# Optimization experiments

Hardware: AMD Instinct MI355X
Metric: run time of the kernel (lower is better)

Reference implementation:

```python
import jax, jax.numpy as jnp
import numpy as np

B, N = 8, 256            # molecules, atoms per molecule (equal sizes)
BN = B * N               # total nodes
E = 16384                # total edges
H, NH, HD = 256, 8, 32   # hidden, heads, head_dim
VD = 8                   # (lmax+1)^2 - 1 with lmax=2
CUTOFF = 5.0


def setup_inputs() -> dict:
    key = jax.random.key(0)
    ks = jax.random.split(key, 24)
    s = 1.0 / np.sqrt(H)
    d_raw = jax.random.normal(ks[5], (E, VD), jnp.float32)
    d_ij = d_raw / (jnp.linalg.norm(d_raw, axis=1, keepdims=True) + 1e-8)
    return {
        'x': jax.random.normal(ks[0], (BN, H), jnp.float32),
        'vec': jax.random.normal(ks[1], (BN, VD, H), jnp.float32),
        'edge_index': jax.random.randint(ks[2], (2, E), 0, BN, jnp.int32),
        'r_ij': jax.random.uniform(ks[3], (E,), jnp.float32) * CUTOFF,
        'f_ij': jax.random.normal(ks[4], (E, H), jnp.float32),
        'd_ij': d_ij,
        'batch': jnp.arange(BN, dtype=jnp.int32) // N,
        'ln_w': jnp.ones((H,), jnp.float32),
        'ln_b': jnp.zeros((H,), jnp.float32),
        'Wq': jax.random.normal(ks[6], (H, H), jnp.float32) * s,
        'Wk': jax.random.normal(ks[7], (H, H), jnp.float32) * s,
        'Wv': jax.random.normal(ks[8], (H, H), jnp.float32) * s,
        'Wao': jax.random.normal(ks[9], (H, H), jnp.float32) * s,
        'Wvec': jax.random.normal(ks[10], (H, 2 * H), jnp.float32) * s,
        'Wdv': jax.random.normal(ks[11], (H, H), jnp.float32) * s,
        'bdv': jnp.zeros((H,), jnp.float32),
        'Ws': jax.random.normal(ks[12], (H, 2 * H), jnp.float32) * s,
        'bs': jnp.zeros((2 * H,), jnp.float32),
        'Wo': jax.random.normal(ks[13], (H, 3 * H), jnp.float32) * s,
        'bo': jnp.zeros((3 * H,), jnp.float32),
        'Wf': jax.random.normal(ks[14], (H, H), jnp.float32) * s,
        'bf': jnp.zeros((H,), jnp.float32),
        'Wsrc': jax.random.normal(ks[15], (H, H), jnp.float32) * s,
        'Wtrg': jax.random.normal(ks[16], (H, H), jnp.float32) * s,
    }


def _vector_rejection(v, d):
    # v: [E, VD, H], d: [E, VD]
    proj = (v * d[:, :, None]).sum(axis=1, keepdims=True)
    return v - proj * d[:, :, None]


def _layer(x, vec, edge_index, r_ij, f_ij, d_ij,
           ln_w, ln_b, Wq, Wk, Wv, Wao, Wvec, Wdv, bdv,
           Ws, bs, Wo, bo, Wf, bf, Wsrc, Wtrg):
    silu = jax.nn.silu
    # ---- LayerNorm on scalar features; VecLayerNorm('none', non-trainable) = identity
    mu = x.mean(-1, keepdims=True)
    var = ((x - mu) ** 2).mean(-1, keepdims=True)
    xn = (x - mu) / jnp.sqrt(var + 1e-5) * ln_w + ln_b

    # ---- 3-body padded attention (equal graph sizes -> mask is all-True)
    x_x = xn.reshape(B, N, H)
    q = (x_x @ Wq).reshape(B, N, NH, HD)
    k = (x_x @ Wk).reshape(B, N, NH, HD)
    vv = (x_x @ Wv).reshape(B, N, NH, HD)
    attn = silu(jnp.einsum('bihd,bjhd->bhij', q, k) / jnp.sqrt(jnp.float32(HD)))
    # mean over neighbor dim j fused into the contraction ( / N )
    v = (jnp.einsum('bhij,bjhd->bihd', attn, vv) / N).reshape(B, N, H) @ Wao
    v = v.reshape(BN, NH, HD)

    dv = silu(f_ij @ Wdv + bdv).reshape(E, NH, HD)
    vp = vec @ Wvec                       # [BN, VD, 2H]
    vec1, vec3 = vp[..., :H], vp[..., H:]
    vec_sum = vec1.sum(axis=1)            # [BN, H]

    # ---- message passing (source_to_target: gather at src, scatter-add at dst)
    src, dst = edge_index[0], edge_index[1]
    cut = 0.5 * (jnp.cos(jnp.pi * r_ij / CUTOFF) + 1.0) * (r_ij < CUTOFF)
    v_j = (v[src] * cut[:, None, None] * dv).reshape(E, H)
    s12 = silu(v_j @ Ws + bs)
    s1, s2 = s12[:, :H], s12[:, H:]
    vec_j = vec[src] * s1[:, None, :] + s2[:, None, :] * d_ij[:, :, None]
    x_agg = jax.ops.segment_sum(v_j, dst, num_segments=BN)
    vec_agg = jax.ops.segment_sum(vec_j, dst, num_segments=BN)

    o = x_agg @ Wo + bo
    o1, o2, o3 = o[:, :H], o[:, H:2 * H], o[:, 2 * H:]
    dx = vec_sum * o2 + o3
    dvec = vec3 * o1[:, None, :] + vec_agg

    # ---- edge update (not last layer)
    w1 = _vector_rejection(vec[dst] @ Wtrg, d_ij)
    w2 = _vector_rejection(vec[src] @ Wsrc, -d_ij)
    w_dot = (w1 * w2).sum(axis=1)         # [E, H]
    df_ij = silu(f_ij @ Wf + bf) * w_dot
    return dx, dvec, df_ij


def reference(x, vec, edge_index, r_ij, f_ij, d_ij, batch,
              ln_w, ln_b, Wq, Wk, Wv, Wao, Wvec, Wdv, bdv,
              Ws, bs, Wo, bo, Wf, bf, Wsrc, Wtrg):
    return _layer(x, vec, edge_index, r_ij, f_ij, d_ij,
                  ln_w, ln_b, Wq, Wk, Wv, Wao, Wvec, Wdv, bdv,
                  Ws, bs, Wo, bo, Wf, bf, Wsrc, Wtrg)
```

## Files before the change

kernel.cpp:

```cpp
#include <hip/hip_runtime.h>
#include <hip/hip_bf16.h>
#include <math.h>

typedef __hip_bfloat16 bf16;
#define DEV __device__ __forceinline__
DEV float silu_f(float x) { return x / (1.0f + __expf(-x)); }
DEV float toF(bf16 x) { return __bfloat162float(x); }
DEV void storeF(float* p, float v) { *p = v; }
DEV void storeF(bf16* p, float v) { *p = __float2bfloat16(v); }

constexpr int Bc = 8, Nc = 256, BNc = 2048, Ec = 16384;
constexpr int Hc = 256, NHc = 8, HDc = 32, VDc = 8;

typedef __attribute__((ext_vector_type(8))) short short8;
typedef __attribute__((ext_vector_type(4))) float floatx4;

DEV void async_copy16(const void* g, void* l) {
  __builtin_amdgcn_global_load_lds(
      (const __attribute__((address_space(1))) void*)g,
      (__attribute__((address_space(3))) void*)l, 16, 0, 0);
}

__global__ __launch_bounds__(1024) void csr_k(const int* __restrict__ ei,
                                              int* __restrict__ rowptr,
                                              int* __restrict__ eids) {
  __shared__ int deg[2048];
  __shared__ int cur[2048];
  __shared__ int ps[1024];
  __shared__ int rp[2048];
  int t = threadIdx.x;
  for (int i = t; i < 2048; i += 1024) { deg[i] = 0; cur[i] = 0; }
  __syncthreads();
  for (int e = t; e < Ec; e += 1024) atomicAdd(&deg[ei[Ec + e]], 1);
  __syncthreads();
  int s0 = deg[2 * t], s1 = deg[2 * t + 1];
  ps[t] = s0 + s1;
  __syncthreads();
  for (int off = 1; off < 1024; off <<= 1) {
    int v = (t >= off) ? ps[t - off] : 0;
    __syncthreads();
    ps[t] += v;
    __syncthreads();
  }
  int base = (t == 0) ? 0 : ps[t - 1];
  rp[2 * t] = base; rp[2 * t + 1] = base + s0;
  rowptr[2 * t] = base; rowptr[2 * t + 1] = base + s0;
  if (t == 1023) rowptr[2048] = Ec;
  __syncthreads();
  for (int e = t; e < Ec; e += 1024) {
    int d = ei[Ec + e];
    int p = atomicAdd(&cur[d], 1);
    eids[rp[d] + p] = e;
  }
}

struct WDesc { const float* in; bf16* out; int K, N; };
struct WAll { WDesc d[11]; };

__global__ __launch_bounds__(256) void wprep_all_k(WAll wa) {
  WDesc wd = wa.d[blockIdx.z];
  if ((int)blockIdx.y * 32 >= wd.N) return;
  __shared__ float t[32][33];
  int k0 = blockIdx.x * 32, n0 = blockIdx.y * 32;
  int tx = threadIdx.x & 31, ty = threadIdx.x >> 5;
#pragma unroll
  for (int i = 0; i < 32; i += 8)
    t[ty + i][tx] = wd.in[(size_t)(k0 + ty + i) * wd.N + n0 + tx];
  __syncthreads();
#pragma unroll
  for (int i = 0; i < 32; i += 8)
    wd.out[(size_t)(n0 + ty + i) * wd.K + k0 + tx] = __float2bfloat16(t[tx][ty + i]);
}

__global__ __launch_bounds__(256) void cvt2_k(const float* __restrict__ a,
                                              bf16* __restrict__ ao,
                                              const float* __restrict__ b,
                                              bf16* __restrict__ bo) {
  int blk = blockIdx.x;
  const float* in = (blk < 4096) ? a : b;
  bf16* out = (blk < 4096) ? ao : bo;
  int i = ((blk & 4095) * 256 + threadIdx.x) * 4;
  float4 v = *(const float4*)&in[i];
  union { bf16 x[4]; uint2 u; } o;
  o.x[0] = __float2bfloat16(v.x); o.x[1] = __float2bfloat16(v.y);
  o.x[2] = __float2bfloat16(v.z); o.x[3] = __float2bfloat16(v.w);
  *(uint2*)&out[i] = o.u;
}

__global__ __launch_bounds__(256) void ln_k(const float* __restrict__ x,
    const float* __restrict__ w, const float* __restrict__ b,
    bf16* __restrict__ xn) {
  int row = blockIdx.x, h = threadIdx.x;
  float v = x[(size_t)row * Hc + h];
  __shared__ float sm[256];
  sm[h] = v; __syncthreads();
  for (int s = 128; s > 0; s >>= 1) { if (h < s) sm[h] += sm[h + s]; __syncthreads(); }
  float mu = sm[0] * (1.0f / 256.0f);
  __syncthreads();
  float d = v - mu;
  sm[h] = d * d; __syncthreads();
  for (int s = 128; s > 0; s >>= 1) { if (h < s) sm[h] += sm[h + s]; __syncthreads(); }
  float var = sm[0] * (1.0f / 256.0f);
  float r = rsqrtf(var + 1e-5f);
  xn[(size_t)row * Hc + h] = __float2bfloat16(d * r * w[h] + b[h]);
}

template <int ACT, typename TC>
__global__ __launch_bounds__(256) void mgemm_k(
    const bf16* __restrict__ A, const bf16* __restrict__ Bt,
    const float* __restrict__ bias, TC* __restrict__ C,
    int M, int K, int N) {
  __shared__ bf16 Als[128 * 32];
  __shared__ bf16 Bls[128 * 32];
  int tid = threadIdx.x;
  int lane = tid & 63, w = tid >> 6;
  int m0 = blockIdx.x * 128, n0 = blockIdx.y * 128;
  int wm = (w & 1) * 64, wn = (w >> 1) * 64;
  int fm = lane & 15, g = lane >> 4;
  floatx4 acc[4][4] = {};
  for (int k0 = 0; k0 < K; k0 += 32) {
#pragma unroll
    for (int t = 0; t < 2; ++t) {
      int c = t * 256 + w * 64 + lane;
      int r = c >> 2, q = c & 3;
      bf16* ldsA = &Als[(t * 256 + w * 64) * 8 + lane * 8];
      bf16* ldsB = &Bls[(t * 256 + w * 64) * 8 + lane * 8];
      async_copy16(A + (size_t)(m0 + r) * K + k0 + q * 8, ldsA);
      async_copy16(Bt + (size_t)(n0 + r) * K + k0 + q * 8, ldsB);
    }
    __syncthreads();
    short8 af[4], bg[4];
#pragma unroll
    for (int i = 0; i < 4; ++i) {
      af[i] = *(const short8*)&Als[(wm + i * 16 + fm) * 32 + g * 8];
      bg[i] = *(const short8*)&Bls[(wn + i * 16 + fm) * 32 + g * 8];
    }
#pragma unroll
    for (int mi = 0; mi < 4; ++mi)
#pragma unroll
      for (int ni = 0; ni < 4; ++ni)
        acc[mi][ni] = __builtin_amdgcn_mfma_f32_16x16x32_bf16(
            af[mi], bg[ni], acc[mi][ni], 0, 0, 0);
    __syncthreads();
  }
#pragma unroll
  for (int mi = 0; mi < 4; ++mi) {
    int row0 = m0 + wm + mi * 16 + g * 4;
#pragma unroll
    for (int ni = 0; ni < 4; ++ni) {
      int col = n0 + wn + ni * 16 + fm;
      float bv = bias ? bias[col] : 0.0f;
#pragma unroll
      for (int r = 0; r < 4; ++r) {
        float v = acc[mi][ni][r] + bv;
        if (ACT) v = silu_f(v);
        storeF(&C[(size_t)(row0 + r) * N + col], v);
      }
    }
  }
}

__global__ __launch_bounds__(256) void gemm_dvfw_k(
    const bf16* __restrict__ A, const bf16* __restrict__ Bt,
    const float* __restrict__ bdv, const float* __restrict__ bf_,
    const int* __restrict__ ei, const float* __restrict__ r_ij,
    const float* __restrict__ vbuf,
    bf16* __restrict__ vj, bf16* __restrict__ fW) {
  constexpr int K = 256, N = 512;
  __shared__ bf16 Als[128 * 32];
  __shared__ bf16 Bls[128 * 32];
  int tid = threadIdx.x;
  int lane = tid & 63, w = tid >> 6;
  int m0 = blockIdx.x * 128, n0 = blockIdx.y * 128;
  int wm = (w & 1) * 64, wn = (w >> 1) * 64;
  int fm = lane & 15, g = lane >> 4;
  floatx4 acc[4][4] = {};
  for (int k0 = 0; k0 < K; k0 += 32) {
#pragma unroll
    for (int t = 0; t < 2; ++t) {
      int c = t * 256 + w * 64 + lane;
      int r = c >> 2, q = c & 3;
      bf16* ldsA = &Als[(t * 256 + w * 64) * 8 + lane * 8];
      bf16* ldsB = &Bls[(t * 256 + w * 64) * 8 + lane * 8];
      async_copy16(A + (size_t)(m0 + r) * K + k0 + q * 8, ldsA);
      async_copy16(Bt + (size_t)(n0 + r) * K + k0 + q * 8, ldsB);
    }
    __syncthreads();
    short8 af[4], bg[4];
#pragma unroll
    for (int i = 0; i < 4; ++i) {
      af[i] = *(const short8*)&Als[(wm + i * 16 + fm) * 32 + g * 8];
      bg[i] = *(const short8*)&Bls[(wn + i * 16 + fm) * 32 + g * 8];
    }
#pragma unroll
    for (int mi = 0; mi < 4; ++mi)
#pragma unroll
      for (int ni = 0; ni < 4; ++ni)
        acc[mi][ni] = __builtin_amdgcn_mfma_f32_16x16x32_bf16(
            af[mi], bg[ni], acc[mi][ni], 0, 0, 0);
    __syncthreads();
  }
  bool isVj = (n0 < 256);
#pragma unroll
  for (int mi = 0; mi < 4; ++mi) {
    int row0 = m0 + wm + mi * 16 + g * 4;
#pragma unroll
    for (int r = 0; r < 4; ++r) {
      int e = row0 + r;
      int src = 0; float cut = 0.f;
      if (isVj) {
        src = ei[e];
        float rr = r_ij[e];
        cut = (rr < 5.0f) ? 0.5f * (cosf(0.6283185307179586f * rr) + 1.0f) : 0.0f;
      }
#pragma unroll
      for (int ni = 0; ni < 4; ++ni) {
        int col = n0 + wn + ni * 16 + fm;
        if (isVj) {
          float v = silu_f(acc[mi][ni][r] + bdv[col]);
          vj[(size_t)e * 256 + col] =
              __float2bfloat16(vbuf[(size_t)src * 256 + col] * cut * v);
        } else {
          float v = silu_f(acc[mi][ni][r] + bf_[col - 256]);
          fW[(size_t)e * 256 + (col - 256)] = __float2bfloat16(v);
        }
      }
    }
  }
}

__global__ __launch_bounds__(256) void attn_mfma_k(
    const bf16* __restrict__ qkv, bf16* __restrict__ ob) {
  constexpr int QS = 768;
  int b = blockIdx.x >> 3, h = blockIdx.x & 7;
  int tid = threadIdx.x, lane = tid & 63, w = tid >> 6;
  int fm = lane & 15, g = lane >> 4;
  __shared__ bf16 Vt[32][264];
  __shared__ bf16 Ps[4][64][72];
  const bf16* qb = qkv + (size_t)b * 256 * QS + h * 32;
  const bf16* kb = qb + 256;
  const bf16* vb = qb + 512;
#pragma unroll
  for (int c = 0; c < 4; ++c) {
    int chunk = c * 256 + tid;
    int j = chunk >> 2, part = chunk & 3;
    union { short8 v; bf16 x[8]; } t;
    t.v = *(const short8*)(vb + (size_t)j * QS + part * 8);
#pragma unroll
    for (int i = 0; i < 8; ++i) Vt[part * 8 + i][j] = t.x[i];
  }
  __syncthreads();
  short8 af[4];
#pragma unroll
  for (int mi = 0; mi < 4; ++mi)
    af[mi] = *(const short8*)(qb + (size_t)(w * 64 + mi * 16 + fm) * QS + g * 8);
  floatx4 oacc[4][2] = {};
  for (int jt = 0; jt < 4; ++jt) {
#pragma unroll
    for (int ni = 0; ni < 4; ++ni) {
      short8 bg = *(const short8*)(kb + (size_t)(jt * 64 + ni * 16 + fm) * QS + g * 8);
#pragma unroll
      for (int mi = 0; mi < 4; ++mi) {
        floatx4 z = {0.f, 0.f, 0.f, 0.f};
        floatx4 s = __builtin_amdgcn_mfma_f32_16x16x32_bf16(af[mi], bg, z, 0, 0, 0);
#pragma unroll
        for (int r = 0; r < 4; ++r) {
          float v = silu_f(s[r] * 0.17677669529663687f);
          Ps[w][mi * 16 + g * 4 + r][ni * 16 + fm] = __float2bfloat16(v);
        }
      }
    }
#pragma unroll
    for (int kt = 0; kt < 2; ++kt) {
      short8 bv0 = *(const short8*)&Vt[fm][jt * 64 + kt * 32 + g * 8];
      short8 bv1 = *(const short8*)&Vt[16 + fm][jt * 64 + kt * 32 + g * 8];
#pragma unroll
      for (int mi = 0; mi < 4; ++mi) {
        short8 ap = *(const short8*)&Ps[w][mi * 16 + fm][kt * 32 + g * 8];
        oacc[mi][0] = __builtin_amdgcn_mfma_f32_16x16x32_bf16(ap, bv0, oacc[mi][0], 0, 0, 0);
        oacc[mi][1] = __builtin_amdgcn_mfma_f32_16x16x32_bf16(ap, bv1, oacc[mi][1], 0, 0, 0);
      }
    }
  }
#pragma unroll
  for (int mi = 0; mi < 4; ++mi)
#pragma unroll
    for (int ni = 0; ni < 2; ++ni)
#pragma unroll
      for (int r = 0; r < 4; ++r) {
        int row = w * 64 + mi * 16 + g * 4 + r;
        int d = ni * 16 + fm;
        ob[((size_t)(b * 256 + row)) * 256 + h * 32 + d] =
            __float2bfloat16(oacc[mi][ni][r] * (1.0f / 256.0f));
      }
}

__global__ __launch_bounds__(256) void xagg_k(const bf16* __restrict__ vj,
                                              const int* __restrict__ rowptr,
                                              const int* __restrict__ eids,
                                              bf16* __restrict__ xagg_bf) {
  int n = blockIdx.x, h = threadIdx.x;
  float acc = 0.f;
  int lo = rowptr[n], hi = rowptr[n + 1];
  for (int i = lo; i < hi; ++i) {
    int e = eids[i];
    acc += toF(vj[(size_t)e * Hc + h]);
  }
  xagg_bf[(size_t)n * Hc + h] = __float2bfloat16(acc);
}

__global__ __launch_bounds__(256) void dvec_agg_k(
    const bf16* __restrict__ vec_bf, const bf16* __restrict__ s12,
    const float* __restrict__ d_ij, const int* __restrict__ ei,
    const int* __restrict__ rowptr, const int* __restrict__ eids,
    const bf16* __restrict__ vpT, const float* __restrict__ o,
    float* __restrict__ out) {
  int n = blockIdx.x, h = threadIdx.x;
  float acc[8] = {};
  int lo = rowptr[n], hi = rowptr[n + 1];
  for (int i = lo; i < hi; ++i) {
    int e = eids[i];
    int src = ei[e];
    float s1 = toF(s12[(size_t)e * 512 + h]);
    float s2 = toF(s12[(size_t)e * 512 + 256 + h]);
#pragma unroll
    for (int vd = 0; vd < 8; ++vd) {
      float dd = d_ij[(size_t)e * VDc + vd];
      acc[vd] += toF(vec_bf[((size_t)src * VDc + vd) * Hc + h]) * s1 + s2 * dd;
    }
  }
  float o1 = o[(size_t)n * 768 + h];
#pragma unroll
  for (int vd = 0; vd < 8; ++vd) {
    float v3 = toF(vpT[((size_t)n * VDc + vd) * 1024 + 256 + h]);
    out[((size_t)n * VDc + vd) * Hc + h] = v3 * o1 + acc[vd];
  }
}

__global__ __launch_bounds__(256) void dxsum_k(const bf16* __restrict__ vpT,
                                               const float* __restrict__ o,
                                               float* __restrict__ out) {
  int idx = blockIdx.x * 256 + threadIdx.x;
  int row = idx >> 8, col = idx & 255;
  float s = 0.f;
#pragma unroll
  for (int vd = 0; vd < 8; ++vd)
    s += toF(vpT[((size_t)row * 8 + vd) * 1024 + col]);
  float o2 = o[(size_t)row * 768 + 256 + col];
  float o3 = o[(size_t)row * 768 + 512 + col];
  out[idx] = s * o2 + o3;
}

__global__ __launch_bounds__(256) void df_k(
    const bf16* __restrict__ vpT, const float* __restrict__ d_ij,
    const bf16* __restrict__ fW, const int* __restrict__ ei,
    float* __restrict__ out) {
  int e = blockIdx.x, h = threadIdx.x;
  int src = ei[e], dst = ei[Ec + e];
  float S = 0.f, p1 = 0.f, p2 = 0.f;
#pragma unroll
  for (int vd = 0; vd < 8; ++vd) {
    float t1 = toF(vpT[((size_t)dst * 8 + vd) * 1024 + 512 + h]);
    float t2 = toF(vpT[((size_t)src * 8 + vd) * 1024 + 768 + h]);
    float dd = d_ij[(size_t)e * 8 + vd];
    S += t1 * t2; p1 += t1 * dd; p2 += t2 * dd;
  }
  out[(size_t)e * Hc + h] = toF(fW[(size_t)e * Hc + h]) * (S - p1 * p2);
}

extern "C" void kernel_launch(void* const* d_in, const int* in_sizes, int n_in,
                              void* d_out, int out_size, void* d_ws, size_t ws_size,
                              hipStream_t stream) {
  const float* x    = (const float*)d_in[0];
  const float* vec  = (const float*)d_in[1];
  const int*   ei   = (const int*)d_in[2];
  const float* r_ij = (const float*)d_in[3];
  const float* f_ij = (const float*)d_in[4];
  const float* d_ij = (const float*)d_in[5];
  const float* ln_w = (const float*)d_in[7];
  const float* ln_b = (const float*)d_in[8];
  const float* Wq   = (const float*)d_in[9];
  const float* Wk   = (const float*)d_in[10];
  const float* Wv   = (const float*)d_in[11];
  const float* Wao  = (const float*)d_in[12];
  const float* Wvec = (const float*)d_in[13];
  const float* Wdv  = (const float*)d_in[14];
  const float* bdv  = (const float*)d_in[15];
  const float* Ws   = (const float*)d_in[16];
  const float* bs   = (const float*)d_in[17];
  const float* Wo   = (const float*)d_in[18];
  const float* bo   = (const float*)d_in[19];
  const float* Wf   = (const float*)d_in[20];
  const float* bf_  = (const float*)d_in[21];
  const float* Wsrc = (const float*)d_in[22];
  const float* Wtrg = (const float*)d_in[23];

  char* p = (char*)d_ws;
  auto alloc = [&](size_t bytes) {
    char* r = p; p += (bytes + 255) & ~(size_t)255; return r;
  };
  bf16*  xn_bf   = (bf16*)alloc((size_t)BNc * Hc * 2);
  bf16*  qkv_bf  = (bf16*)alloc((size_t)BNc * 3 * Hc * 2);
  bf16*  attn_bf = (bf16*)alloc((size_t)BNc * Hc * 2);
  float* vbuf    = (float*)alloc((size_t)BNc * Hc * 4);
  bf16*  xagg_bf = (bf16*)alloc((size_t)BNc * Hc * 2);
  float* obuf    = (float*)alloc((size_t)BNc * 3 * Hc * 4);
  bf16*  f_bf    = (bf16*)alloc((size_t)Ec * Hc * 2);
  bf16*  vec_bf  = (bf16*)alloc((size_t)BNc * VDc * Hc * 2);
  bf16*  vpT     = (bf16*)alloc((size_t)Ec * 1024 * 2);
  bf16*  vj_bf   = (bf16*)alloc((size_t)Ec * Hc * 2);
  bf16*  s12_bf  = (bf16*)alloc((size_t)Ec * 2 * Hc * 2);
  bf16*  fW_bf   = (bf16*)alloc((size_t)Ec * Hc * 2);
  bf16*  Wqkv_t  = (bf16*)alloc((size_t)3 * Hc * Hc * 2);
  bf16*  Wao_t   = (bf16*)alloc((size_t)Hc * Hc * 2);
  bf16*  Wdvf_t  = (bf16*)alloc((size_t)2 * Hc * Hc * 2);
  bf16*  Wvt_t   = (bf16*)alloc((size_t)4 * Hc * Hc * 2);
  bf16*  Ws_t    = (bf16*)alloc((size_t)2 * Hc * Hc * 2);
  bf16*  Wo_t    = (bf16*)alloc((size_t)3 * Hc * Hc * 2);
  int*   rowptr  = (int*)alloc(2049 * 4);
  int*   eids    = (int*)alloc(Ec * 4);

  float* out_dx   = (float*)d_out;
  float* out_dvec = (float*)d_out + 524288;
  float* out_df   = (float*)d_out + 4718592;

  csr_k<<<1, 1024, 0, stream>>>(ei, rowptr, eids);

  WAll wa;
  wa.d[0]  = {Wq,   Wqkv_t,           Hc, Hc};
  wa.d[1]  = {Wk,   Wqkv_t + 65536,   Hc, Hc};
  wa.d[2]  = {Wv,   Wqkv_t + 131072,  Hc, Hc};
  wa.d[3]  = {Wao,  Wao_t,            Hc, Hc};
  wa.d[4]  = {Wdv,  Wdvf_t,           Hc, Hc};
  wa.d[5]  = {Wf,   Wdvf_t + 65536,   Hc, Hc};
  wa.d[6]  = {Wvec, Wvt_t,            Hc, 2 * Hc};
  wa.d[7]  = {Wtrg, Wvt_t + 131072,   Hc, Hc};
  wa.d[8]  = {Wsrc, Wvt_t + 196608,   Hc, Hc};
  wa.d[9]  = {Ws,   Ws_t,             Hc, 2 * Hc};
  wa.d[10] = {Wo,   Wo_t,             Hc, 3 * Hc};
  wprep_all_k<<<dim3(8, 24, 11), 256, 0, stream>>>(wa);

  cvt2_k<<<8192, 256, 0, stream>>>(f_ij, f_bf, vec, vec_bf);

  ln_k<<<BNc, 256, 0, stream>>>(x, ln_w, ln_b, xn_bf);

  mgemm_k<0, bf16><<<dim3(16, 6), 256, 0, stream>>>(xn_bf, Wqkv_t, nullptr, qkv_bf, BNc, Hc, 3 * Hc);

  attn_mfma_k<<<Bc * NHc, 256, 0, stream>>>(qkv_bf, attn_bf);

  mgemm_k<0, float><<<dim3(16, 2), 256, 0, stream>>>(attn_bf, Wao_t, nullptr, vbuf, BNc, Hc, Hc);

  mgemm_k<0, bf16><<<dim3(128, 8), 256, 0, stream>>>(vec_bf, Wvt_t, nullptr, vpT, Ec, Hc, 4 * Hc);

  gemm_dvfw_k<<<dim3(128, 4), 256, 0, stream>>>(f_bf, Wdvf_t, bdv, bf_, ei, r_ij,
                                                vbuf, vj_bf, fW_bf);

  xagg_k<<<BNc, 256, 0, stream>>>(vj_bf, rowptr, eids, xagg_bf);

  mgemm_k<1, bf16><<<dim3(128, 4), 256, 0, stream>>>(vj_bf, Ws_t, bs, s12_bf, Ec, Hc, 2 * Hc);

  mgemm_k<0, float><<<dim3(16, 6), 256, 0, stream>>>(xagg_bf, Wo_t, bo, obuf, BNc, Hc, 3 * Hc);

  dxsum_k<<<2048, 256, 0, stream>>>(vpT, obuf, out_dx);

  dvec_agg_k<<<BNc, 256, 0, stream>>>(vec_bf, s12_bf, d_ij, ei, rowptr, eids,
                                      vpT, obuf, out_dvec);

  df_k<<<Ec, 256, 0, stream>>>(vpT, d_ij, fW_bf, ei, out_df);

  (void)in_sizes; (void)n_in; (void)out_size; (void)ws_size;
}
```

Measured before the change: 326.8 us.

## Merge independent stages into horizontally fused kernels and vectorize gather kernels

```diff
diff --git a/kernel.cpp b/kernel.cpp
--- a/kernel.cpp
+++ b/kernel.cpp
@@ -14,6 +14,7 @@
 
 typedef __attribute__((ext_vector_type(8))) short short8;
 typedef __attribute__((ext_vector_type(4))) float floatx4;
+union sh8 { short8 v; bf16 x[8]; };
 
 DEV void async_copy16(const void* g, void* l) {
   __builtin_amdgcn_global_load_lds(
@@ -21,33 +22,38 @@
       (__attribute__((address_space(3))) void*)l, 16, 0, 0);
 }
 
-__global__ __launch_bounds__(1024) void csr_k(const int* __restrict__ ei,
-                                              int* __restrict__ rowptr,
-                                              int* __restrict__ eids) {
-  __shared__ int deg[2048];
-  __shared__ int cur[2048];
-  __shared__ int ps[1024];
-  __shared__ int rp[2048];
+
+DEV void csr_body(const int* __restrict__ ei, int* __restrict__ rowptr,
+                  int* __restrict__ eids, int* sm) {
+  int* deg = sm;
+  int* cur = sm + 2048;
+  int* rp  = sm + 4096;
+  int* ps  = sm + 6144;
   int t = threadIdx.x;
-  for (int i = t; i < 2048; i += 1024) { deg[i] = 0; cur[i] = 0; }
-  __syncthreads();
-  for (int e = t; e < Ec; e += 1024) atomicAdd(&deg[ei[Ec + e]], 1);
-  __syncthreads();
-  int s0 = deg[2 * t], s1 = deg[2 * t + 1];
-  ps[t] = s0 + s1;
-  __syncthreads();
-  for (int off = 1; off < 1024; off <<= 1) {
+  for (int i = t; i < 2048; i += 256) { deg[i] = 0; cur[i] = 0; }
+  __syncthreads();
+  for (int e = t; e < Ec; e += 256) atomicAdd(&deg[ei[Ec + e]], 1);
+  __syncthreads();
+  int loc[8], s = 0;
+#pragma unroll
+  for (int i = 0; i < 8; ++i) { loc[i] = s; s += deg[t * 8 + i]; }
+  ps[t] = s;
+  __syncthreads();
+  for (int off = 1; off < 256; off <<= 1) {
     int v = (t >= off) ? ps[t - off] : 0;
     __syncthreads();
     ps[t] += v;
     __syncthreads();
   }
   int base = (t == 0) ? 0 : ps[t - 1];
-  rp[2 * t] = base; rp[2 * t + 1] = base + s0;
-  rowptr[2 * t] = base; rowptr[2 * t + 1] = base + s0;
-  if (t == 1023) rowptr[2048] = Ec;
-  __syncthreads();
-  for (int e = t; e < Ec; e += 1024) {
+#pragma unroll
+  for (int i = 0; i < 8; ++i) {
+    rp[t * 8 + i] = base + loc[i];
+    rowptr[t * 8 + i] = base + loc[i];
+  }
+  if (t == 255) rowptr[2048] = Ec;
+  __syncthreads();
+  for (int e = t; e < Ec; e += 256) {
     int d = ei[Ec + e];
     int p = atomicAdd(&cur[d], 1);
     eids[rp[d] + p] = e;
@@ -55,13 +61,11 @@
 }
 
 struct WDesc { const float* in; bf16* out; int K, N; };
-struct WAll { WDesc d[11]; };
-
-__global__ __launch_bounds__(256) void wprep_all_k(WAll wa) {
-  WDesc wd = wa.d[blockIdx.z];
-  if ((int)blockIdx.y * 32 >= wd.N) return;
-  __shared__ float t[32][33];
-  int k0 = blockIdx.x * 32, n0 = blockIdx.y * 32;
+
+DEV void wprep_body(WDesc wd, int by, int bx, float* sm) {
+  if (by * 32 >= wd.N) return;
+  float (*t)[33] = (float (*)[33])sm;
+  int k0 = bx * 32, n0 = by * 32;
   int tx = threadIdx.x & 31, ty = threadIdx.x >> 5;
 #pragma unroll
   for (int i = 0; i < 32; i += 8)
@@ -72,14 +76,8 @@
     wd.out[(size_t)(n0 + ty + i) * wd.K + k0 + tx] = __float2bfloat16(t[tx][ty + i]);
 }
 
-__global__ __launch_bounds__(256) void cvt2_k(const float* __restrict__ a,
-                                              bf16* __restrict__ ao,
-                                              const float* __restrict__ b,
-                                              bf16* __restrict__ bo) {
-  int blk = blockIdx.x;
-  const float* in = (blk < 4096) ? a : b;
-  bf16* out = (blk < 4096) ? ao : bo;
-  int i = ((blk & 4095) * 256 + threadIdx.x) * 4;
+DEV void cvt_body(const float* __restrict__ in, bf16* __restrict__ out, int blk) {
+  int i = (blk * 256 + threadIdx.x) * 4;
   float4 v = *(const float4*)&in[i];
   union { bf16 x[4]; uint2 u; } o;
   o.x[0] = __float2bfloat16(v.x); o.x[1] = __float2bfloat16(v.y);
@@ -87,12 +85,11 @@
   *(uint2*)&out[i] = o.u;
 }
 
-__global__ __launch_bounds__(256) void ln_k(const float* __restrict__ x,
-    const float* __restrict__ w, const float* __restrict__ b,
-    bf16* __restrict__ xn) {
-  int row = blockIdx.x, h = threadIdx.x;
+DEV void ln_body(const float* __restrict__ x, const float* __restrict__ w,
+                 const float* __restrict__ b, bf16* __restrict__ xn,
+                 int row, float* sm) {
+  int h = threadIdx.x;
   float v = x[(size_t)row * Hc + h];
-  __shared__ float sm[256];
   sm[h] = v; __syncthreads();
   for (int s = 128; s > 0; s >>= 1) { if (h < s) sm[h] += sm[h + s]; __syncthreads(); }
   float mu = sm[0] * (1.0f / 256.0f);
@@ -106,15 +103,12 @@
 }
 
 template <int ACT, typename TC>
-__global__ __launch_bounds__(256) void mgemm_k(
-    const bf16* __restrict__ A, const bf16* __restrict__ Bt,
-    const float* __restrict__ bias, TC* __restrict__ C,
-    int M, int K, int N) {
-  __shared__ bf16 Als[128 * 32];
-  __shared__ bf16 Bls[128 * 32];
+DEV void mgemm_body(const bf16* __restrict__ A, const bf16* __restrict__ Bt,
+                    const float* __restrict__ bias, TC* __restrict__ C,
+                    int M, int K, int N, int m0, int n0,
+                    bf16* Als, bf16* Bls) {
   int tid = threadIdx.x;
   int lane = tid & 63, w = tid >> 6;
-  int m0 = blockIdx.x * 128, n0 = blockIdx.y * 128;
   int wm = (w & 1) * 64, wn = (w >> 1) * 64;
   int fm = lane & 15, g = lane >> 4;
   floatx4 acc[4][4] = {};
@@ -160,15 +154,237 @@
   }
 }
 
+DEV void xagg_body(const bf16* __restrict__ vj, const int* __restrict__ rowptr,
+                   const int* __restrict__ eids, bf16* __restrict__ xagg, int blk) {
+  int node = blk * 8 + (threadIdx.x >> 5);
+  int tx = threadIdx.x & 31;
+  float acc[8] = {};
+  int lo = rowptr[node], hi = rowptr[node + 1];
+  for (int i = lo; i < hi; ++i) {
+    sh8 vv; vv.v = *(const short8*)&vj[(size_t)eids[i] * 256 + tx * 8];
+#pragma unroll
+    for (int c = 0; c < 8; ++c) acc[c] += toF(vv.x[c]);
+  }
+  sh8 o;
+#pragma unroll
+  for (int c = 0; c < 8; ++c) o.x[c] = __float2bfloat16(acc[c]);
+  *(short8*)&xagg[(size_t)node * 256 + tx * 8] = o.v;
+}
+
+DEV void df_body(const bf16* __restrict__ vpT, const float* __restrict__ d_ij,
+                 const bf16* __restrict__ fW, const int* __restrict__ ei,
+                 float* __restrict__ out, int blk) {
+  int te = threadIdx.x >> 5, tx = threadIdx.x & 31;
+  int e = blk * 8 + te;
+  int src = ei[e], dst = ei[Ec + e];
+  float S[8] = {}, p1[8] = {}, p2[8] = {};
+#pragma unroll
+  for (int vd = 0; vd < 8; ++vd) {
+    sh8 t1, t2;
+    t1.v = *(const short8*)&vpT[((size_t)(dst * 8 + vd)) * 1024 + 512 + tx * 8];
+    t2.v = *(const short8*)&vpT[((size_t)(src * 8 + vd)) * 1024 + 768 + tx * 8];
+    float dd = d_ij[e * 8 + vd];
+#pragma unroll
+    for (int c = 0; c < 8; ++c) {
+      float a = toF(t1.x[c]), b = toF(t2.x[c]);
+      S[c] += a * b; p1[c] += a * dd; p2[c] += b * dd;
+    }
+  }
+  sh8 fw; fw.v = *(const short8*)&fW[(size_t)e * 256 + tx * 8];
+  float o[8];
+#pragma unroll
+  for (int c = 0; c < 8; ++c) o[c] = toF(fw.x[c]) * (S[c] - p1[c] * p2[c]);
+  float* dst_p = &out[(size_t)e * 256 + tx * 8];
+  *(float4*)dst_p = make_float4(o[0], o[1], o[2], o[3]);
+  *(float4*)(dst_p + 4) = make_float4(o[4], o[5], o[6], o[7]);
+}
+
+DEV void dxsum_body(const bf16* __restrict__ vpT, const float* __restrict__ ob,
+                    float* __restrict__ out, int blk) {
+  int row = blk * 8 + (threadIdx.x >> 5);
+  int tx = threadIdx.x & 31;
+  float s[8] = {};
+#pragma unroll
+  for (int vd = 0; vd < 8; ++vd) {
+    sh8 vv; vv.v = *(const short8*)&vpT[((size_t)(row * 8 + vd)) * 1024 + tx * 8];
+#pragma unroll
+    for (int c = 0; c < 8; ++c) s[c] += toF(vv.x[c]);
+  }
+  float4 o2a = *(const float4*)&ob[(size_t)row * 768 + 256 + tx * 8];
+  float4 o2b = *(const float4*)&ob[(size_t)row * 768 + 260 + tx * 8];
+  float4 o3a = *(const float4*)&ob[(size_t)row * 768 + 512 + tx * 8];
+  float4 o3b = *(const float4*)&ob[(size_t)row * 768 + 516 + tx * 8];
+  float o2[8] = {o2a.x, o2a.y, o2a.z, o2a.w, o2b.x, o2b.y, o2b.z, o2b.w};
+  float o3[8] = {o3a.x, o3a.y, o3a.z, o3a.w, o3b.x, o3b.y, o3b.z, o3b.w};
+  float r[8];
+#pragma unroll
+  for (int c = 0; c < 8; ++c) r[c] = s[c] * o2[c] + o3[c];
+  float* dp = &out[(size_t)row * 256 + tx * 8];
+  *(float4*)dp = make_float4(r[0], r[1], r[2], r[3]);
+  *(float4*)(dp + 4) = make_float4(r[4], r[5], r[6], r[7]);
+}
+
+DEV void dvec_body(const bf16* __restrict__ vec_bf, const bf16* __restrict__ s12,
+                   const float* __restrict__ d_ij, const int* __restrict__ ei,
+                   const int* __restrict__ rowptr, const int* __restrict__ eids,
+                   const bf16* __restrict__ vpT, const float* __restrict__ ob,
+                   float* __restrict__ out, int n) {
+  int tv = threadIdx.x >> 5, tx = threadIdx.x & 31;
+  float acc[8] = {};
+  int lo = rowptr[n], hi = rowptr[n + 1];
+  for (int i = lo; i < hi; ++i) {
+    int e = eids[i];
+    int src = ei[e];
+    sh8 s1, s2, vv;
+    s1.v = *(const short8*)&s12[(size_t)e * 512 + tx * 8];
+    s2.v = *(const short8*)&s12[(size_t)e * 512 + 256 + tx * 8];
+    vv.v = *(const short8*)&vec_bf[((size_t)(src * 8 + tv)) * 256 + tx * 8];
+    float dd = d_ij[e * 8 + tv];
+#pragma unroll
+    for (int c = 0; c < 8; ++c)
+      acc[c] += toF(vv.x[c]) * toF(s1.x[c]) + toF(s2.x[c]) * dd;
+  }
+  sh8 v3; v3.v = *(const short8*)&vpT[((size_t)(n * 8 + tv)) * 1024 + 256 + tx * 8];
+  float4 o1a = *(const float4*)&ob[(size_t)n * 768 + tx * 8];
+  float4 o1b = *(const float4*)&ob[(size_t)n * 768 + 4 + tx * 8];
+  float o1[8] = {o1a.x, o1a.y, o1a.z, o1a.w, o1b.x, o1b.y, o1b.z, o1b.w};
+  float r[8];
+#pragma unroll
+  for (int c = 0; c < 8; ++c) r[c] = toF(v3.x[c]) * o1[c] + acc[c];
+  float* dp = &out[((size_t)(n * 8 + tv)) * 256 + tx * 8];
+  *(float4*)dp = make_float4(r[0], r[1], r[2], r[3]);
+  *(float4*)(dp + 4) = make_float4(r[4], r[5], r[6], r[7]);
+}
+
+
+struct PrepArgs {
+  const int* ei; int* rowptr; int* eids;
+  WDesc wd[11];
+  const float* f_ij; bf16* f_bf;
+  const float* vec; bf16* vec_bf;
+  const float* x; const float* ln_w; const float* ln_b; bf16* xn;
+};
+
+__global__ __launch_bounds__(256) void prep_k(PrepArgs a) {
+  __shared__ __align__(16) char smem[25600];
+  int blk = blockIdx.x;
+  if (blk == 0) { csr_body(a.ei, a.rowptr, a.eids, (int*)smem); return; }
+  blk -= 1;
+  if (blk < 2112) { wprep_body(a.wd[blk / 192], (blk % 192) / 8, blk % 8, (float*)smem); return; }
+  blk -= 2112;
+  if (blk < 8192) {
+    if (blk < 4096) cvt_body(a.f_ij, a.f_bf, blk);
+    else cvt_body(a.vec, a.vec_bf, blk - 4096);
+    return;
+  }
+  blk -= 8192;
+  ln_body(a.x, a.ln_w, a.ln_b, a.xn, blk, (float*)smem);
+}
+
+struct G2Args {
+  const bf16 *xn, *Wqkv, *vecbf, *Wvt;
+  bf16 *qkv, *vpT;
+};
+__global__ __launch_bounds__(256) void gemm2_k(G2Args a) {
+  __shared__ __align__(16) char smem[16384];
+  bf16* Als = (bf16*)smem; bf16* Bls = (bf16*)(smem + 8192);
+  int id = blockIdx.x;
+  if (id < 96)
+    mgemm_body<0, bf16>(a.xn, a.Wqkv, nullptr, a.qkv, BNc, Hc, 768,
+                        (id % 16) * 128, (id / 16) * 128, Als, Bls);
+  else {
+    id -= 96;
+    mgemm_body<0, bf16>(a.vecbf, a.Wvt, nullptr, a.vpT, Ec, Hc, 1024,
+                        (id % 128) * 128, (id / 128) * 128, Als, Bls);
+  }
+}
+
+__global__ __launch_bounds__(256) void attn_mfma_k(
+    const bf16* __restrict__ qkv, bf16* __restrict__ ob) {
+  constexpr int QS = 768;
+  int b = blockIdx.x >> 3, h = blockIdx.x & 7;
+  int tid = threadIdx.x, lane = tid & 63, w = tid >> 6;
+  int fm = lane & 15, g = lane >> 4;
+  __shared__ bf16 Vt[32][264];
+  __shared__ bf16 Ps[4][64][72];
+  const bf16* qb = qkv + (size_t)b * 256 * QS + h * 32;
+  const bf16* kb = qb + 256;
+  const bf16* vb = qb + 512;
+#pragma unroll
+  for (int c = 0; c < 4; ++c) {
+    int chunk = c * 256 + tid;
+    int j = chunk >> 2, part = chunk & 3;
+    sh8 t;
+    t.v = *(const short8*)(vb + (size_t)j * QS + part * 8);
+#pragma unroll
+    for (int i = 0; i < 8; ++i) Vt[part * 8 + i][j] = t.x[i];
+  }
+  __syncthreads();
+  short8 af[4];
+#pragma unroll
+  for (int mi = 0; mi < 4; ++mi)
+    af[mi] = *(const short8*)(qb + (size_t)(w * 64 + mi * 16 + fm) * QS + g * 8);
+  floatx4 oacc[4][2] = {};
+  for (int jt = 0; jt < 4; ++jt) {
+#pragma unroll
+    for (int ni = 0; ni < 4; ++ni) {
+      short8 bg = *(const short8*)(kb + (size_t)(jt * 64 + ni * 16 + fm) * QS + g * 8);
+#pragma unroll
+      for (int mi = 0; mi < 4; ++mi) {
+        floatx4 z = {0.f, 0.f, 0.f, 0.f};
+        floatx4 s = __builtin_amdgcn_mfma_f32_16x16x32_bf16(af[mi], bg, z, 0, 0, 0);
+#pragma unroll
+        for (int r = 0; r < 4; ++r) {
+          float v = silu_f(s[r] * 0.17677669529663687f);
+          Ps[w][mi * 16 + g * 4 + r][ni * 16 + fm] = __float2bfloat16(v);
+        }
+      }
+    }
+#pragma unroll
+    for (int kt = 0; kt < 2; ++kt) {
+      short8 bv0 = *(const short8*)&Vt[fm][jt * 64 + kt * 32 + g * 8];
+      short8 bv1 = *(const short8*)&Vt[16 + fm][jt * 64 + kt * 32 + g * 8];
+#pragma unroll
+      for (int mi = 0; mi < 4; ++mi) {
+        short8 ap = *(const short8*)&Ps[w][mi * 16 + fm][kt * 32 + g * 8];
+        oacc[mi][0] = __builtin_amdgcn_mfma_f32_16x16x32_bf16(ap, bv0, oacc[mi][0], 0, 0, 0);
+        oacc[mi][1] = __builtin_amdgcn_mfma_f32_16x16x32_bf16(ap, bv1, oacc[mi][1], 0, 0, 0);
+      }
+    }
+  }
+#pragma unroll
+  for (int mi = 0; mi < 4; ++mi)
+#pragma unroll
+    for (int ni = 0; ni < 2; ++ni)
+#pragma unroll
+      for (int r = 0; r < 4; ++r) {
+        int row = w * 64 + mi * 16 + g * 4 + r;
+        int d = ni * 16 + fm;
+        ob[((size_t)(b * 256 + row)) * 256 + h * 32 + d] =
+            __float2bfloat16(oacc[mi][ni][r] * (1.0f / 256.0f));
+      }
+}
+
+template <int ACT, typename TC>
+__global__ __launch_bounds__(256) void mgemm_k(
+    const bf16* __restrict__ A, const bf16* __restrict__ Bt,
+    const float* __restrict__ bias, TC* __restrict__ C,
+    int M, int K, int N) {
+  __shared__ __align__(16) char smem[16384];
+  mgemm_body<ACT, TC>(A, Bt, bias, C, M, K, N,
+                      blockIdx.x * 128, blockIdx.y * 128,
+                      (bf16*)smem, (bf16*)(smem + 8192));
+}
+
 __global__ __launch_bounds__(256) void gemm_dvfw_k(
     const bf16* __restrict__ A, const bf16* __restrict__ Bt,
     const float* __restrict__ bdv, const float* __restrict__ bf_,
     const int* __restrict__ ei, const float* __restrict__ r_ij,
     const float* __restrict__ vbuf,
     bf16* __restrict__ vj, bf16* __restrict__ fW) {
-  constexpr int K = 256, N = 512;
-  __shared__ bf16 Als[128 * 32];
-  __shared__ bf16 Bls[128 * 32];
+  constexpr int K = 256;
+  __shared__ __align__(16) char smem[16384];
+  bf16* Als = (bf16*)smem; bf16* Bls = (bf16*)(smem + 8192);
   int tid = threadIdx.x;
   int lane = tid & 63, w = tid >> 6;
   int m0 = blockIdx.x * 128, n0 = blockIdx.y * 128;
@@ -229,143 +445,49 @@
   }
 }
 
-__global__ __launch_bounds__(256) void attn_mfma_k(
-    const bf16* __restrict__ qkv, bf16* __restrict__ ob) {
-  constexpr int QS = 768;
-  int b = blockIdx.x >> 3, h = blockIdx.x & 7;
-  int tid = threadIdx.x, lane = tid & 63, w = tid >> 6;
-  int fm = lane & 15, g = lane >> 4;
-  __shared__ bf16 Vt[32][264];
-  __shared__ bf16 Ps[4][64][72];
-  const bf16* qb = qkv + (size_t)b * 256 * QS + h * 32;
-  const bf16* kb = qb + 256;
-  const bf16* vb = qb + 512;
-#pragma unroll
-  for (int c = 0; c < 4; ++c) {
-    int chunk = c * 256 + tid;
-    int j = chunk >> 2, part = chunk & 3;
-    union { short8 v; bf16 x[8]; } t;
-    t.v = *(const short8*)(vb + (size_t)j * QS + part * 8);
-#pragma unroll
-    for (int i = 0; i < 8; ++i) Vt[part * 8 + i][j] = t.x[i];
-  }
-  __syncthreads();
-  short8 af[4];
-#pragma unroll
-  for (int mi = 0; mi < 4; ++mi)
-    af[mi] = *(const short8*)(qb + (size_t)(w * 64 + mi * 16 + fm) * QS + g * 8);
-  floatx4 oacc[4][2] = {};
-  for (int jt = 0; jt < 4; ++jt) {
-#pragma unroll
-    for (int ni = 0; ni < 4; ++ni) {
-      short8 bg = *(const short8*)(kb + (size_t)(jt * 64 + ni * 16 + fm) * QS + g * 8);
-#pragma unroll
-      for (int mi = 0; mi < 4; ++mi) {
-        floatx4 z = {0.f, 0.f, 0.f, 0.f};
-        floatx4 s = __builtin_amdgcn_mfma_f32_16x16x32_bf16(af[mi], bg, z, 0, 0, 0);
-#pragma unroll
-        for (int r = 0; r < 4; ++r) {
-          float v = silu_f(s[r] * 0.17677669529663687f);
-          Ps[w][mi * 16 + g * 4 + r][ni * 16 + fm] = __float2bfloat16(v);
-        }
-      }
-    }
-#pragma unroll
-    for (int kt = 0; kt < 2; ++kt) {
-      short8 bv0 = *(const short8*)&Vt[fm][jt * 64 + kt * 32 + g * 8];
-      short8 bv1 = *(const short8*)&Vt[16 + fm][jt * 64 + kt * 32 + g * 8];
-#pragma unroll
-      for (int mi = 0; mi < 4; ++mi) {
-        short8 ap = *(const short8*)&Ps[w][mi * 16 + fm][kt * 32 + g * 8];
-        oacc[mi][0] = __builtin_amdgcn_mfma_f32_16x16x32_bf16(ap, bv0, oacc[mi][0], 0, 0, 0);
-        oacc[mi][1] = __builtin_amdgcn_mfma_f32_16x16x32_bf16(ap, bv1, oacc[mi][1], 0, 0, 0);
-      }
-    }
-  }
-#pragma unroll
-  for (int mi = 0; mi < 4; ++mi)
-#pragma unroll
-    for (int ni = 0; ni < 2; ++ni)
-#pragma unroll
-      for (int r = 0; r < 4; ++r) {
-        int row = w * 64 + mi * 16 + g * 4 + r;
-        int d = ni * 16 + fm;
-        ob[((size_t)(b * 256 + row)) * 256 + h * 32 + d] =
-            __float2bfloat16(oacc[mi][ni][r] * (1.0f / 256.0f));
-      }
-}
-
-__global__ __launch_bounds__(256) void xagg_k(const bf16* __restrict__ vj,
-                                              const int* __restrict__ rowptr,
-                                              const int* __restrict__ eids,
-                                              bf16* __restrict__ xagg_bf) {
-  int n = blockIdx.x, h = threadIdx.x;
-  float acc = 0.f;
-  int lo = rowptr[n], hi = rowptr[n + 1];
-  for (int i = lo; i < hi; ++i) {
-    int e = eids[i];
-    acc += toF(vj[(size_t)e * Hc + h]);
-  }
-  xagg_bf[(size_t)n * Hc + h] = __float2bfloat16(acc);
-}
-
-__global__ __launch_bounds__(256) void dvec_agg_k(
-    const bf16* __restrict__ vec_bf, const bf16* __restrict__ s12,
-    const float* __restrict__ d_ij, const int* __restrict__ ei,
-    const int* __restrict__ rowptr, const int* __restrict__ eids,
-    const bf16* __restrict__ vpT, const float* __restrict__ o,
-    float* __restrict__ out) {
-  int n = blockIdx.x, h = threadIdx.x;
-  float acc[8] = {};
-  int lo = rowptr[n], hi = rowptr[n + 1];
-  for (int i = lo; i < hi; ++i) {
-    int e = eids[i];
-    int src = ei[e];
-    float s1 = toF(s12[(size_t)e * 512 + h]);
-    float s2 = toF(s12[(size_t)e * 512 + 256 + h]);
-#pragma unroll
-    for (int vd = 0; vd < 8; ++vd) {
-      float dd = d_ij[(size_t)e * VDc + vd];
-      acc[vd] += toF(vec_bf[((size_t)src * VDc + vd) * Hc + h]) * s1 + s2 * dd;
-    }
-  }
-  float o1 = o[(size_t)n * 768 + h];
-#pragma unroll
-  for (int vd = 0; vd < 8; ++vd) {
-    float v3 = toF(vpT[((size_t)n * VDc + vd) * 1024 + 256 + h]);
-    out[((size_t)n * VDc + vd) * Hc + h] = v3 * o1 + acc[vd];
-  }
-}
-
-__global__ __launch_bounds__(256) void dxsum_k(const bf16* __restrict__ vpT,
-                                               const float* __restrict__ o,
-                                               float* __restrict__ out) {
-  int idx = blockIdx.x * 256 + threadIdx.x;
-  int row = idx >> 8, col = idx & 255;
-  float s = 0.f;
-#pragma unroll
-  for (int vd = 0; vd < 8; ++vd)
-    s += toF(vpT[((size_t)row * 8 + vd) * 1024 + col]);
-  float o2 = o[(size_t)row * 768 + 256 + col];
-  float o3 = o[(size_t)row * 768 + 512 + col];
-  out[idx] = s * o2 + o3;
-}
-
-__global__ __launch_bounds__(256) void df_k(
-    const bf16* __restrict__ vpT, const float* __restrict__ d_ij,
-    const bf16* __restrict__ fW, const int* __restrict__ ei,
-    float* __restrict__ out) {
-  int e = blockIdx.x, h = threadIdx.x;
-  int src = ei[e], dst = ei[Ec + e];
-  float S = 0.f, p1 = 0.f, p2 = 0.f;
-#pragma unroll
-  for (int vd = 0; vd < 8; ++vd) {
-    float t1 = toF(vpT[((size_t)dst * 8 + vd) * 1024 + 512 + h]);
-    float t2 = toF(vpT[((size_t)src * 8 + vd) * 1024 + 768 + h]);
-    float dd = d_ij[(size_t)e * 8 + vd];
-    S += t1 * t2; p1 += t1 * dd; p2 += t2 * dd;
-  }
-  out[(size_t)e * Hc + h] = toF(fW[(size_t)e * Hc + h]) * (S - p1 * p2);
+struct S6Args {
+  const bf16 *vj, *Ws_t; const float* bs; bf16* s12;
+  const int *rowptr, *eids; bf16* xagg;
+};
+__global__ __launch_bounds__(256) void stage6_k(S6Args a) {
+  __shared__ __align__(16) char smem[16384];
+  int id = blockIdx.x;
+  if (id < 512)
+    mgemm_body<1, bf16>(a.vj, a.Ws_t, a.bs, a.s12, Ec, Hc, 512,
+                        (id % 128) * 128, (id / 128) * 128,
+                        (bf16*)smem, (bf16*)(smem + 8192));
+  else
+    xagg_body(a.vj, a.rowptr, a.eids, a.xagg, id - 512);
+}
+
+struct S7Args {
+  const bf16 *xagg, *Wo_t; const float* bo; float* obuf;
+  const bf16* vpT; const float* d_ij; const bf16* fW;
+  const int* ei; float* out_df;
+};
+__global__ __launch_bounds__(256) void stage7_k(S7Args a) {
+  __shared__ __align__(16) char smem[16384];
+  int id = blockIdx.x;
+  if (id < 96)
+    mgemm_body<0, float>(a.xagg, a.Wo_t, a.bo, a.obuf, BNc, Hc, 768,
+                         (id % 16) * 128, (id / 16) * 128,
+                         (bf16*)smem, (bf16*)(smem + 8192));
+  else
+    df_body(a.vpT, a.d_ij, a.fW, a.ei, a.out_df, id - 96);
+}
+
+struct S8Args {
+  const bf16* vpT; const float* obuf; float* out_dx;
+  const bf16 *vecbf, *s12; const float* d_ij;
+  const int *ei, *rowptr, *eids; float* out_dvec;
+};
+__global__ __launch_bounds__(256) void stage8_k(S8Args a) {
+  int id = blockIdx.x;
+  if (id < 256)
+    dxsum_body(a.vpT, a.obuf, a.out_dx, id);
+  else
+    dvec_body(a.vecbf, a.s12, a.d_ij, a.ei, a.rowptr, a.eids,
+              a.vpT, a.obuf, a.out_dvec, id - 256);
 }
 
 extern "C" void kernel_launch(void* const* d_in, const int* in_sizes, int n_in,
@@ -424,49 +546,41 @@
   float* out_dvec = (float*)d_out + 524288;
   float* out_df   = (float*)d_out + 4718592;
 
-  csr_k<<<1, 1024, 0, stream>>>(ei, rowptr, eids);
-
-  WAll wa;
-  wa.d[0]  = {Wq,   Wqkv_t,           Hc, Hc};
-  wa.d[1]  = {Wk,   Wqkv_t + 65536,   Hc, Hc};
-  wa.d[2]  = {Wv,   Wqkv_t + 131072,  Hc, Hc};
-  wa.d[3]  = {Wao,  Wao_t,            Hc, Hc};
-  wa.d[4]  = {Wdv,  Wdvf_t,           Hc, Hc};
-  wa.d[5]  = {Wf,   Wdvf_t + 65536,   Hc, Hc};
-  wa.d[6]  = {Wvec, Wvt_t,            Hc, 2 * Hc};
-  wa.d[7]  = {Wtrg, Wvt_t + 131072,   Hc, Hc};
-  wa.d[8]  = {Wsrc, Wvt_t + 196608,   Hc, Hc};
-  wa.d[9]  = {Ws,   Ws_t,             Hc, 2 * Hc};
-  wa.d[10] = {Wo,   Wo_t,             Hc, 3 * Hc};
-  wprep_all_k<<<dim3(8, 24, 11), 256, 0, stream>>>(wa);
-
-  cvt2_k<<<8192, 256, 0, stream>>>(f_ij, f_bf, vec, vec_bf);
-
-  ln_k<<<BNc, 256, 0, stream>>>(x, ln_w, ln_b, xn_bf);
-
-  mgemm_k<0, bf16><<<dim3(16, 6), 256, 0, stream>>>(xn_bf, Wqkv_t, nullptr, qkv_bf, BNc, Hc, 3 * Hc);
+  PrepArgs pa;
+  pa.ei = ei; pa.rowptr = rowptr; pa.eids = eids;
+  pa.wd[0]  = {Wq,   Wqkv_t,           Hc, Hc};
+  pa.wd[1]  = {Wk,   Wqkv_t + 65536,   Hc, Hc};
+  pa.wd[2]  = {Wv,   Wqkv_t + 131072,  Hc, Hc};
+  pa.wd[3]  = {Wao,  Wao_t,            Hc, Hc};
+  pa.wd[4]  = {Wdv,  Wdvf_t,           Hc, Hc};
+  pa.wd[5]  = {Wf,   Wdvf_t + 65536,   Hc, Hc};
+  pa.wd[6]  = {Wvec, Wvt_t,            Hc, 2 * Hc};
+  pa.wd[7]  = {Wtrg, Wvt_t + 131072,   Hc, Hc};
+  pa.wd[8]  = {Wsrc, Wvt_t + 196608,   Hc, Hc};
+  pa.wd[9]  = {Ws,   Ws_t,             Hc, 2 * Hc};
+  pa.wd[10] = {Wo,   Wo_t,             Hc, 3 * Hc};
+  pa.f_ij = f_ij; pa.f_bf = f_bf; pa.vec = vec; pa.vec_bf = vec_bf;
+  pa.x = x; pa.ln_w = ln_w; pa.ln_b = ln_b; pa.xn = xn_bf;
+  prep_k<<<12353, 256, 0, stream>>>(pa);
+
+  G2Args g2{xn_bf, Wqkv_t, vec_bf, Wvt_t, qkv_bf, vpT};
+  gemm2_k<<<1120, 256, 0, stream>>>(g2);
 
   attn_mfma_k<<<Bc * NHc, 256, 0, stream>>>(qkv_bf, attn_bf);
 
   mgemm_k<0, float><<<dim3(16, 2), 256, 0, stream>>>(attn_bf, Wao_t, nullptr, vbuf, BNc, Hc, Hc);
-
-  mgemm_k<0, bf16><<<dim3(128, 8), 256, 0, stream>>>(vec_bf, Wvt_t, nullptr, vpT, Ec, Hc, 4 * Hc);
 
   gemm_dvfw_k<<<dim3(128, 4), 256, 0, stream>>>(f_bf, Wdvf_t, bdv, bf_, ei, r_ij,
                                                 vbuf, vj_bf, fW_bf);
 
-  xagg_k<<<BNc, 256, 0, stream>>>(vj_bf, rowptr, eids, xagg_bf);
-
-  mgemm_k<1, bf16><<<dim3(128, 4), 256, 0, stream>>>(vj_bf, Ws_t, bs, s12_bf, Ec, Hc, 2 * Hc);
-
-  mgemm_k<0, float><<<dim3(16, 6), 256, 0, stream>>>(xagg_bf, Wo_t, bo, obuf, BNc, Hc, 3 * Hc);
-
-  dxsum_k<<<2048, 256, 0, stream>>>(vpT, obuf, out_dx);
-
-  dvec_agg_k<<<BNc, 256, 0, stream>>>(vec_bf, s12_bf, d_ij, ei, rowptr, eids,
-                                      vpT, obuf, out_dvec);
-
-  df_k<<<Ec, 256, 0, stream>>>(vpT, d_ij, fW_bf, ei, out_df);
+  S6Args s6{vj_bf, Ws_t, bs, s12_bf, rowptr, eids, xagg_bf};
+  stage6_k<<<768, 256, 0, stream>>>(s6);
+
+  S7Args s7{xagg_bf, Wo_t, bo, obuf, vpT, d_ij, fW_bf, ei, out_df};
+  stage7_k<<<2144, 256, 0, stream>>>(s7);
+
+  S8Args s8{vpT, obuf, out_dx, vec_bf, s12_bf, d_ij, ei, rowptr, eids, out_dvec};
+  stage8_k<<<2304, 256, 0, stream>>>(s8);
 
   (void)in_sizes; (void)n_in; (void)out_size; (void)ws_size;
 }
```

After: 302.6 us. -7.4%, faster.
